# Kernel optimization log

Hardware: AMD Instinct MI355X
Metric: run time of the kernel (lower is better)

The kernel has to match this reference:

```python
import jax, jax.numpy as jnp
import numpy as np

B, T, H, L, O = 128, 1024, 256, 2, 256

def setup_inputs() -> dict:
    key = jax.random.key(0)
    ks = jax.random.split(key, 8)
    s = 1.0 / np.sqrt(H)
    return {
        "encoder_outputs": jax.random.normal(ks[0], (B, T, H), jnp.float32),
        "encoder_hidden": jax.random.normal(ks[1], (L, B, H), jnp.float32),
        "W_ih": jax.random.normal(ks[2], (L, 3 * H, H), jnp.float32) * s,
        "W_hh": jax.random.normal(ks[3], (L, 3 * H, H), jnp.float32) * s,
        "b_ih": jax.random.normal(ks[4], (L, 3 * H), jnp.float32) * s,
        "b_hh": jax.random.normal(ks[5], (L, 3 * H), jnp.float32) * s,
        "W_out": jax.random.normal(ks[6], (O, H), jnp.float32) * s,
        "b_out": jax.random.normal(ks[7], (O,), jnp.float32) * s,
    }

def _gru_cell(x, h, Wih, Whh, bih, bhh):
    # PyTorch GRU cell math
    gi = x @ Wih.T + bih          # [B, 3H]
    gh = h @ Whh.T + bhh          # [B, 3H]
    ir, iz, inn = jnp.split(gi, 3, axis=-1)
    hr, hz, hn = jnp.split(gh, 3, axis=-1)
    r = jax.nn.sigmoid(ir + hr)
    z = jax.nn.sigmoid(iz + hz)
    n = jnp.tanh(inn + r * hn)
    return (1.0 - z) * n + z * h

def reference(encoder_outputs, encoder_hidden, W_ih, W_hh, b_ih, b_hh, W_out, b_out):
    b, t, h_dim = encoder_outputs.shape
    n_layers = encoder_hidden.shape[0]

    def step(carry, _):
        h, x = carry                      # h: [L,B,H], x: [B,H]
        inp = x
        new_h = []
        for l in range(n_layers):         # small fixed layer loop
            hl = _gru_cell(inp, h[l], W_ih[l], W_hh[l], b_ih[l], b_hh[l])
            new_h.append(hl)
            inp = hl
        h = jnp.stack(new_h)
        out = inp @ W_out.T + b_out       # [B,O] per-step Linear
        nxt = jax.lax.stop_gradient(out[:, :h_dim])  # .detach() feedback
        return (h, nxt), out

    x0 = jnp.zeros((b, h_dim), encoder_outputs.dtype)
    (h_final, _), outs = jax.lax.scan(step, (encoder_hidden, x0), None, length=t)
    decoder_outputs = jnp.transpose(outs, (1, 0, 2))  # [B,T,O]
    return decoder_outputs, h_final
```

## Files before the change

kernel.cpp:

```cpp
#include <hip/hip_runtime.h>

#define NB 128
#define NT 1024
#define NH 256
#define NL 2
#define NO 256
#define G3 768

#define WIHT_OFF 0
#define WHHT_OFF 393216
#define WOUT_OFF 786432

__global__ void prep_kernel(const float* __restrict__ Wih,
                            const float* __restrict__ Whh,
                            const float* __restrict__ Wout,
                            float* __restrict__ ws) {
  int idx = blockIdx.x * 256 + threadIdx.x;
  if (idx < 393216) {
    int c = idx & 3;
    int q = idx >> 2;
    int j = q % 768;
    int lk4 = q / 768;
    int k4 = lk4 & 63;
    int l = lk4 >> 6;
    size_t src = (size_t)(l * 768 + j) * 256 + k4 * 4 + c;
    ws[WIHT_OFF + idx] = Wih[src];
    ws[WHHT_OFF + idx] = Whh[src];
  }
  if (idx < 65536) {
    int c = idx & 3;
    int q = idx >> 2;
    int o = q & 255;
    int k4 = q >> 8;
    ws[WOUT_OFF + idx] = Wout[o * 256 + k4 * 4 + c];
  }
}

__device__ __forceinline__ float dot4(float4 a, float4 b) {
  return a.x * b.x + a.y * b.y + a.z * b.z + a.w * b.w;
}

__global__ __launch_bounds__(512) void decoder_kernel(
    const float* __restrict__ eh,
    const float* __restrict__ bih,
    const float* __restrict__ bhh,
    const float* __restrict__ bout,
    const float* __restrict__ ws,
    float* __restrict__ out) {
  __shared__ __align__(16) float xv[2 * NH];
  __shared__ __align__(16) float h0s[2 * NH];
  __shared__ __align__(16) float h1s[2 * NH];
  __shared__ float red[3][128][25];
  __shared__ float sbih[NL * G3];
  __shared__ float sbhh[NL * G3];
  __shared__ float sbout[NO];

  const int tid = threadIdx.x;
  const int jj = tid & 127;
  const int kh = tid >> 7;
  const int r0 = blockIdx.x * 2;

  for (int i = tid; i < NL * G3; i += 512) { sbih[i] = bih[i]; sbhh[i] = bhh[i]; }
  for (int i = tid; i < NO; i += 512) sbout[i] = bout[i];
  for (int i = tid; i < 2 * NH; i += 512) {
    int r = i >> 8, k = i & 255;
    h0s[i] = eh[(size_t)(0 * NB + r0 + r) * NH + k];
    h1s[i] = eh[(size_t)(1 * NB + r0 + r) * NH + k];
    xv[i] = 0.f;
  }
  __syncthreads();

  const int k4beg = kh * 16;

  for (int t = 0; t < NT; ++t) {
    for (int l = 0; l < NL; ++l) {
      const float* xin = (l == 0) ? xv : h0s;
      float* hsrc = (l == 0) ? h0s : h1s;
      const float* Wi = ws + WIHT_OFF + l * 196608;
      const float* Wh = ws + WHHT_OFF + l * 196608;
      float acc[24];
#pragma unroll
      for (int i = 0; i < 24; ++i) acc[i] = 0.f;
#pragma unroll 2
      for (int k4 = k4beg; k4 < k4beg + 16; ++k4) {
        const float4* wri = (const float4*)(Wi + k4 * 3072);
        const float4* wrh = (const float4*)(Wh + k4 * 3072);
        float4 xa = *(const float4*)(xin + k4 * 4);
        float4 xb = *(const float4*)(xin + NH + k4 * 4);
        float4 ha = *(const float4*)(hsrc + k4 * 4);
        float4 hb = *(const float4*)(hsrc + NH + k4 * 4);
#pragma unroll
        for (int p = 0; p < 6; ++p) {
          float4 wi = wri[jj + 128 * p];
          float4 wh = wrh[jj + 128 * p];
          acc[0 * 12 + 0 * 6 + p] += dot4(wi, xa);
          acc[0 * 12 + 1 * 6 + p] += dot4(wh, ha);
          acc[1 * 12 + 0 * 6 + p] += dot4(wi, xb);
          acc[1 * 12 + 1 * 6 + p] += dot4(wh, hb);
        }
      }
      if (kh) {
#pragma unroll
        for (int i = 0; i < 24; ++i) red[kh - 1][jj][i] = acc[i];
      }
      __syncthreads();
      if (kh == 0) {
#pragma unroll
        for (int q = 0; q < 3; ++q)
#pragma unroll
          for (int i = 0; i < 24; ++i) acc[i] += red[q][jj][i];
#pragma unroll
        for (int e = 0; e < 2; ++e) {
          int j0 = jj + 128 * e;
#pragma unroll
          for (int r = 0; r < 2; ++r) {
            float gir = acc[r * 12 + e]     + sbih[l * G3 + j0];
            float giz = acc[r * 12 + e + 2] + sbih[l * G3 + 256 + j0];
            float gin = acc[r * 12 + e + 4] + sbih[l * G3 + 512 + j0];
            float ghr = acc[r * 12 + 6 + e]     + sbhh[l * G3 + j0];
            float ghz = acc[r * 12 + 6 + e + 2] + sbhh[l * G3 + 256 + j0];
            float ghn = acc[r * 12 + 6 + e + 4] + sbhh[l * G3 + 512 + j0];
            float rg = 1.f / (1.f + expf(-(gir + ghr)));
            float zg = 1.f / (1.f + expf(-(giz + ghz)));
            float ng = tanhf(gin + rg * ghn);
            float hold = hsrc[r * NH + j0];
            hsrc[r * NH + j0] = (1.f - zg) * ng + zg * hold;
          }
        }
      }
      __syncthreads();
    }
    {
      const float* Wo = ws + WOUT_OFF;
      float oa[4];
#pragma unroll
      for (int i = 0; i < 4; ++i) oa[i] = 0.f;
#pragma unroll 2
      for (int k4 = k4beg; k4 < k4beg + 16; ++k4) {
        const float4* wro = (const float4*)(Wo + k4 * 1024);
        float4 ha = *(const float4*)(h1s + k4 * 4);
        float4 hb = *(const float4*)(h1s + NH + k4 * 4);
#pragma unroll
        for (int p = 0; p < 2; ++p) {
          float4 w = wro[jj + 128 * p];
          oa[p] += dot4(w, ha);
          oa[p + 2] += dot4(w, hb);
        }
      }
      if (kh) {
#pragma unroll
        for (int i = 0; i < 4; ++i) red[kh - 1][jj][i] = oa[i];
      }
      __syncthreads();
      if (kh == 0) {
#pragma unroll
        for (int q = 0; q < 3; ++q)
#pragma unroll
          for (int i = 0; i < 4; ++i) oa[i] += red[q][jj][i];
#pragma unroll
        for (int p = 0; p < 2; ++p) {
          int o = jj + 128 * p;
          float v0 = oa[p] + sbout[o];
          float v1 = oa[p + 2] + sbout[o];
          out[((size_t)(r0 + 0) * NT + t) * NO + o] = v0;
          out[((size_t)(r0 + 1) * NT + t) * NO + o] = v1;
          xv[o] = v0;
          xv[NH + o] = v1;
        }
      }
      __syncthreads();
    }
  }
  const size_t base = (size_t)NB * NT * NO;
  for (int i = tid; i < 2 * NH; i += 512) {
    int r = i >> 8, k = i & 255;
    out[base + (size_t)(0 * NB + r0 + r) * NH + k] = h0s[i];
    out[base + (size_t)(1 * NB + r0 + r) * NH + k] = h1s[i];
  }
}

extern "C" void kernel_launch(void* const* d_in, const int* in_sizes, int n_in,
                              void* d_out, int out_size, void* d_ws, size_t ws_size,
                              hipStream_t stream) {
  const float* eh   = (const float*)d_in[1];
  const float* Wih  = (const float*)d_in[2];
  const float* Whh  = (const float*)d_in[3];
  const float* bih  = (const float*)d_in[4];
  const float* bhh  = (const float*)d_in[5];
  const float* Wout = (const float*)d_in[6];
  const float* bo   = (const float*)d_in[7];
  float* ws  = (float*)d_ws;
  float* out = (float*)d_out;

  hipLaunchKernelGGL(prep_kernel, dim3(1536), dim3(256), 0, stream, Wih, Whh, Wout, ws);
  hipLaunchKernelGGL(decoder_kernel, dim3(64), dim3(512), 0, stream, eh, bih, bhh, bo, ws, out);
}
```

Measured before the change: 34.32 ms.

## Split each batch pair's hidden dimension across four cooperating blocks with flag sync

The decoder now launches 256 blocks of 1024 threads instead of 64 blocks of 512. Four blocks share each pair of batch rows, and each block computes a 64-wide slice of the hidden and output units. After every GRU layer and the output projection, the blocks swap their slices through global scratch slots, using double-buffered per-step flags and spin waits. This spreads the serial recurrence over more CUs and reduces the weight streaming each block does per step. The cost is three inter-block barrier round trips per timestep. Correctness relies on all 256 blocks being co-resident and on relaxed atomics plus vmcnt waits giving enough memory ordering.

```diff
diff --git a/kernel.cpp b/kernel.cpp
--- a/kernel.cpp
+++ b/kernel.cpp
@@ -5,11 +5,14 @@
 #define NH 256
 #define NL 2
 #define NO 256
-#define G3 768
 
 #define WIHT_OFF 0
 #define WHHT_OFF 393216
 #define WOUT_OFF 786432
+#define XSLOT_OFF 851968
+#define H0SLOT_OFF 917504
+#define H1SLOT_OFF 983040
+#define FLAG_OFF 1048576
 
 __global__ void prep_kernel(const float* __restrict__ Wih,
                             const float* __restrict__ Whh,
@@ -34,149 +37,186 @@
     int k4 = q >> 8;
     ws[WOUT_OFF + idx] = Wout[o * 256 + k4 * 4 + c];
   }
+  if (idx < 1536) {
+    int* flags = (int*)ws + FLAG_OFF;
+    __hip_atomic_store(&flags[idx], 0, __ATOMIC_RELAXED, __HIP_MEMORY_SCOPE_AGENT);
+  }
 }
 
 __device__ __forceinline__ float dot4(float4 a, float4 b) {
   return a.x * b.x + a.y * b.y + a.z * b.z + a.w * b.w;
 }
 
-__global__ __launch_bounds__(512) void decoder_kernel(
+__global__ __launch_bounds__(1024) void decoder_kernel(
     const float* __restrict__ eh,
     const float* __restrict__ bih,
     const float* __restrict__ bhh,
     const float* __restrict__ bout,
-    const float* __restrict__ ws,
+    float* __restrict__ ws,
     float* __restrict__ out) {
-  __shared__ __align__(16) float xv[2 * NH];
+  __shared__ float red[16 * 832];
+  __shared__ __align__(16) float xs[2 * NH];
   __shared__ __align__(16) float h0s[2 * NH];
   __shared__ __align__(16) float h1s[2 * NH];
-  __shared__ float red[3][128][25];
-  __shared__ float sbih[NL * G3];
-  __shared__ float sbhh[NL * G3];
-  __shared__ float sbout[NO];
+  __shared__ float sbias[NL * 2 * 3 * 64];
+  __shared__ float sbo[64];
 
   const int tid = threadIdx.x;
-  const int jj = tid & 127;
-  const int kh = tid >> 7;
-  const int r0 = blockIdx.x * 2;
-
-  for (int i = tid; i < NL * G3; i += 512) { sbih[i] = bih[i]; sbhh[i] = bhh[i]; }
-  for (int i = tid; i < NO; i += 512) sbout[i] = bout[i];
-  for (int i = tid; i < 2 * NH; i += 512) {
+  const int b = blockIdx.x;
+  const int s = (b & 7) >> 1;
+  const int g = (b >> 3) + ((b & 1) << 5);
+  const int r0 = g * 2;
+  const int jj = tid & 63;
+  const int kh = tid >> 6;
+  const int hj = s * 64 + jj;
+
+  float* const xslot = ws + XSLOT_OFF;
+  float* const h0slot = ws + H0SLOT_OFF;
+  float* const h1slot = ws + H1SLOT_OFF;
+  int* const flags = (int*)ws + FLAG_OFF;
+
+  if (tid < 768) {
+    int q = tid >> 6;
+    int gate = q % 3, mat = (q / 3) & 1, l = q / 6;
+    const float* bsrc = mat ? bhh : bih;
+    sbias[tid] = bsrc[l * 768 + gate * 256 + hj];
+  }
+  if (tid < 64) sbo[tid] = bout[hj];
+  for (int i = tid; i < 2 * NH; i += 1024) {
     int r = i >> 8, k = i & 255;
-    h0s[i] = eh[(size_t)(0 * NB + r0 + r) * NH + k];
-    h1s[i] = eh[(size_t)(1 * NB + r0 + r) * NH + k];
-    xv[i] = 0.f;
+    h0s[i] = eh[(size_t)(r0 + r) * NH + k];
+    h1s[i] = eh[(size_t)(NB + r0 + r) * NH + k];
+    xs[i] = 0.f;
   }
   __syncthreads();
 
-  const int k4beg = kh * 16;
+#define WAIT_FLAGS(PH, PARV, TGT)                                              \
+  if (tid < 4 && tid != s) {                                                   \
+    const int fidx = (((PH)*2 + (PARV)) * 64 + g) * 4 + tid;                   \
+    while (__hip_atomic_load(&flags[fidx], __ATOMIC_RELAXED,                   \
+                             __HIP_MEMORY_SCOPE_AGENT) < (TGT))                \
+      __builtin_amdgcn_s_sleep(2);                                             \
+  }                                                                            \
+  __syncthreads();
+
+#define LOAD_FULL(DST, SLOT, PARV)                                             \
+  if (tid < 2 * NH) {                                                          \
+    (DST)[tid] = __hip_atomic_load(&(SLOT)[((PARV)*64 + g) * (2 * NH) + tid],  \
+                                   __ATOMIC_RELAXED, __HIP_MEMORY_SCOPE_AGENT);\
+  }                                                                            \
+  __syncthreads();
+
+#define GRU_PHASE(L, XIN, HVEC, SLOT, PH)                                      \
+  {                                                                            \
+    const float4* Wi = (const float4*)(ws + WIHT_OFF + (L)*196608);            \
+    const float4* Wh = (const float4*)(ws + WHHT_OFF + (L)*196608);            \
+    float acc[12];                                   \
+    _Pragma("unroll") for (int i = 0; i < 12; ++i) acc[i] = 0.f;               \
+    _Pragma("unroll") for (int kq = 0; kq < 4; ++kq) {                         \
+      const int k4 = (kh << 2) + kq;                                           \
+      const float4* wi = Wi + k4 * 768 + hj;                                   \
+      const float4* wh = Wh + k4 * 768 + hj;                                   \
+      float4 xa = *(const float4*)((XIN) + k4 * 4);                            \
+      float4 xb = *(const float4*)((XIN) + NH + k4 * 4);                       \
+      float4 ha = *(const float4*)((HVEC) + k4 * 4);                           \
+      float4 hb = *(const float4*)((HVEC) + NH + k4 * 4);                      \
+      _Pragma("unroll") for (int gate = 0; gate < 3; ++gate) {                 \
+        float4 wiv = wi[gate * 256];                                           \
+        float4 whv = wh[gate * 256];                                           \
+        acc[0 + gate] += dot4(wiv, xa);                                        \
+        acc[3 + gate] += dot4(whv, ha);                                        \
+        acc[6 + gate] += dot4(wiv, xb);                                        \
+        acc[9 + gate] += dot4(whv, hb);                                        \
+      }                                                                        \
+    }                                                                          \
+    _Pragma("unroll") for (int i = 0; i < 12; ++i)                             \
+        red[kh * 832 + jj * 13 + i] = acc[i];                                  \
+    __syncthreads();                                                           \
+    float tot = 0.f;                                                           \
+    if (kh < 12) {                                                             \
+      _Pragma("unroll") for (int q = 0; q < 16; ++q)                           \
+          tot += red[q * 832 + jj * 13 + kh];                                  \
+    }                                                                          \
+    __syncthreads();                                                           \
+    if (kh < 12) red[jj * 13 + kh] = tot;                                      \
+    __syncthreads();                                                           \
+    if (kh < 2) {                                                              \
+      const int r = kh;                                                        \
+      float gir = red[jj * 13 + r * 6 + 0] + sbias[((L)*6 + 0) * 64 + jj];     \
+      float giz = red[jj * 13 + r * 6 + 1] + sbias[((L)*6 + 1) * 64 + jj];     \
+      float gin = red[jj * 13 + r * 6 + 2] + sbias[((L)*6 + 2) * 64 + jj];     \
+      float ghr = red[jj * 13 + r * 6 + 3] + sbias[((L)*6 + 3) * 64 + jj];     \
+      float ghz = red[jj * 13 + r * 6 + 4] + sbias[((L)*6 + 4) * 64 + jj];     \
+      float ghn = red[jj * 13 + r * 6 + 5] + sbias[((L)*6 + 5) * 64 + jj];     \
+      float rg = 1.f / (1.f + expf(-(gir + ghr)));                             \
+      float zg = 1.f / (1.f + expf(-(giz + ghz)));                             \
+      float ng = tanhf(gin + rg * ghn);                                        \
+      float hold = (HVEC)[r * NH + hj];                                        \
+      float hnew = (1.f - zg) * ng + zg * hold;                                \
+      __hip_atomic_store(&(SLOT)[((par * 64 + g) * 2 + r) * NH + hj], hnew,    \
+                         __ATOMIC_RELAXED, __HIP_MEMORY_SCOPE_AGENT);          \
+    }                                                                          \
+    asm volatile("s_waitcnt vmcnt(0)" ::: "memory");                           \
+    __syncthreads();                                                           \
+    if (tid == 0)                                                              \
+      __hip_atomic_store(&flags[(((PH)*2 + par) * 64 + g) * 4 + s], t + 1,     \
+                         __ATOMIC_RELAXED, __HIP_MEMORY_SCOPE_AGENT);          \
+  }
 
   for (int t = 0; t < NT; ++t) {
-    for (int l = 0; l < NL; ++l) {
-      const float* xin = (l == 0) ? xv : h0s;
-      float* hsrc = (l == 0) ? h0s : h1s;
-      const float* Wi = ws + WIHT_OFF + l * 196608;
-      const float* Wh = ws + WHHT_OFF + l * 196608;
-      float acc[24];
+    const int par = t & 1;
+    if (t > 0) {
+      WAIT_FLAGS(2, par ^ 1, t);
+      LOAD_FULL(xs, xslot, par ^ 1);
+    }
+    GRU_PHASE(0, xs, h0s, h0slot, 0);
+    WAIT_FLAGS(0, par, t + 1);
+    LOAD_FULL(h0s, h0slot, par);
+    GRU_PHASE(1, h0s, h1s, h1slot, 1);
+    WAIT_FLAGS(1, par, t + 1);
+    LOAD_FULL(h1s, h1slot, par);
+    {
+      const float4* Wo = (const float4*)(ws + WOUT_OFF);
+      float o0 = 0.f, o1 = 0.f;
 #pragma unroll
-      for (int i = 0; i < 24; ++i) acc[i] = 0.f;
-#pragma unroll 2
-      for (int k4 = k4beg; k4 < k4beg + 16; ++k4) {
-        const float4* wri = (const float4*)(Wi + k4 * 3072);
-        const float4* wrh = (const float4*)(Wh + k4 * 3072);
-        float4 xa = *(const float4*)(xin + k4 * 4);
-        float4 xb = *(const float4*)(xin + NH + k4 * 4);
-        float4 ha = *(const float4*)(hsrc + k4 * 4);
-        float4 hb = *(const float4*)(hsrc + NH + k4 * 4);
-#pragma unroll
-        for (int p = 0; p < 6; ++p) {
-          float4 wi = wri[jj + 128 * p];
-          float4 wh = wrh[jj + 128 * p];
-          acc[0 * 12 + 0 * 6 + p] += dot4(wi, xa);
-          acc[0 * 12 + 1 * 6 + p] += dot4(wh, ha);
-          acc[1 * 12 + 0 * 6 + p] += dot4(wi, xb);
-          acc[1 * 12 + 1 * 6 + p] += dot4(wh, hb);
-        }
-      }
-      if (kh) {
-#pragma unroll
-        for (int i = 0; i < 24; ++i) red[kh - 1][jj][i] = acc[i];
-      }
-      __syncthreads();
-      if (kh == 0) {
-#pragma unroll
-        for (int q = 0; q < 3; ++q)
-#pragma unroll
-          for (int i = 0; i < 24; ++i) acc[i] += red[q][jj][i];
-#pragma unroll
-        for (int e = 0; e < 2; ++e) {
-          int j0 = jj + 128 * e;
-#pragma unroll
-          for (int r = 0; r < 2; ++r) {
-            float gir = acc[r * 12 + e]     + sbih[l * G3 + j0];
-            float giz = acc[r * 12 + e + 2] + sbih[l * G3 + 256 + j0];
-            float gin = acc[r * 12 + e + 4] + sbih[l * G3 + 512 + j0];
-            float ghr = acc[r * 12 + 6 + e]     + sbhh[l * G3 + j0];
-            float ghz = acc[r * 12 + 6 + e + 2] + sbhh[l * G3 + 256 + j0];
-            float ghn = acc[r * 12 + 6 + e + 4] + sbhh[l * G3 + 512 + j0];
-            float rg = 1.f / (1.f + expf(-(gir + ghr)));
-            float zg = 1.f / (1.f + expf(-(giz + ghz)));
-            float ng = tanhf(gin + rg * ghn);
-            float hold = hsrc[r * NH + j0];
-            hsrc[r * NH + j0] = (1.f - zg) * ng + zg * hold;
-          }
-        }
-      }
-      __syncthreads();
-    }
-    {
-      const float* Wo = ws + WOUT_OFF;
-      float oa[4];
-#pragma unroll
-      for (int i = 0; i < 4; ++i) oa[i] = 0.f;
-#pragma unroll 2
-      for (int k4 = k4beg; k4 < k4beg + 16; ++k4) {
-        const float4* wro = (const float4*)(Wo + k4 * 1024);
+      for (int kq = 0; kq < 4; ++kq) {
+        const int k4 = (kh << 2) + kq;
+        float4 w = Wo[k4 * 256 + hj];
         float4 ha = *(const float4*)(h1s + k4 * 4);
         float4 hb = *(const float4*)(h1s + NH + k4 * 4);
+        o0 += dot4(w, ha);
+        o1 += dot4(w, hb);
+      }
+      red[kh * 832 + jj * 13 + 0] = o0;
+      red[kh * 832 + jj * 13 + 1] = o1;
+      __syncthreads();
+      if (kh < 2) {
+        const int r = kh;
+        float tot = 0.f;
 #pragma unroll
-        for (int p = 0; p < 2; ++p) {
-          float4 w = wro[jj + 128 * p];
-          oa[p] += dot4(w, ha);
-          oa[p + 2] += dot4(w, hb);
-        }
+        for (int q = 0; q < 16; ++q) tot += red[q * 832 + jj * 13 + r];
+        float v = tot + sbo[jj];
+        out[((size_t)(r0 + r) * NT + t) * NO + hj] = v;
+        __hip_atomic_store(&xslot[((par * 64 + g) * 2 + r) * NH + hj], v,
+                           __ATOMIC_RELAXED, __HIP_MEMORY_SCOPE_AGENT);
       }
-      if (kh) {
-#pragma unroll
-        for (int i = 0; i < 4; ++i) red[kh - 1][jj][i] = oa[i];
-      }
+      asm volatile("s_waitcnt vmcnt(0)" ::: "memory");
       __syncthreads();
-      if (kh == 0) {
-#pragma unroll
-        for (int q = 0; q < 3; ++q)
-#pragma unroll
-          for (int i = 0; i < 4; ++i) oa[i] += red[q][jj][i];
-#pragma unroll
-        for (int p = 0; p < 2; ++p) {
-          int o = jj + 128 * p;
-          float v0 = oa[p] + sbout[o];
-          float v1 = oa[p + 2] + sbout[o];
-          out[((size_t)(r0 + 0) * NT + t) * NO + o] = v0;
-          out[((size_t)(r0 + 1) * NT + t) * NO + o] = v1;
-          xv[o] = v0;
-          xv[NH + o] = v1;
-        }
-      }
-      __syncthreads();
+      if (tid == 0)
+        __hip_atomic_store(&flags[((2 * 2 + par) * 64 + g) * 4 + s], t + 1,
+                           __ATOMIC_RELAXED, __HIP_MEMORY_SCOPE_AGENT);
     }
   }
-  const size_t base = (size_t)NB * NT * NO;
-  for (int i = tid; i < 2 * NH; i += 512) {
-    int r = i >> 8, k = i & 255;
-    out[base + (size_t)(0 * NB + r0 + r) * NH + k] = h0s[i];
-    out[base + (size_t)(1 * NB + r0 + r) * NH + k] = h1s[i];
-  }
+
+  if (tid < 128) {
+    const int r = tid >> 6;
+    const size_t base = (size_t)NB * NT * NO;
+    out[base + (size_t)(r0 + r) * NH + hj] = h0s[r * NH + hj];
+    out[base + (size_t)(NB + r0 + r) * NH + hj] = h1s[r * NH + hj];
+  }
+#undef WAIT_FLAGS
+#undef LOAD_FULL
+#undef GRU_PHASE
 }
 
 extern "C" void kernel_launch(void* const* d_in, const int* in_sizes, int n_in,
@@ -193,5 +233,6 @@
   float* out = (float*)d_out;
 
   hipLaunchKernelGGL(prep_kernel, dim3(1536), dim3(256), 0, stream, Wih, Whh, Wout, ws);
-  hipLaunchKernelGGL(decoder_kernel, dim3(64), dim3(512), 0, stream, eh, bih, bhh, bo, ws, out);
-}
+  hipLaunchKernelGGL(decoder_kernel, dim3(256), dim3(1024), 0, stream,
+                     eh, bih, bhh, bo, ws, out);
+}
```

Measured after the change: 30.06 ms. -12.4%, faster.
